# Kernel optimization log

Measured on AMD Instinct MI355X. Metric: run time of the kernel, lower is better.

Reference implementation:

```python
import jax, jax.numpy as jnp
import numpy as np

E, T, IN, OUT = 8, 16384, 1024, 1024  # n_groups, total_tokens, in_features, out_features


def setup_inputs() -> dict:
    key = jax.random.key(0)
    kx, kw, ks = jax.random.split(key, 3)
    x = jax.random.normal(kx, (T, IN), dtype=jnp.float32)
    # kaiming_uniform-ish scale for weight [E, OUT, IN]
    weight = jax.random.normal(kw, (E, OUT, IN), dtype=jnp.float32) * (1.0 / np.sqrt(IN))
    # ragged segment lengths that sum exactly to T (random cut points)
    cuts = jnp.sort(jax.random.randint(ks, (E - 1,), 0, T + 1)).astype(jnp.int32)
    seg_lens = jnp.diff(
        jnp.concatenate([jnp.zeros((1,), jnp.int32), cuts, jnp.full((1,), T, jnp.int32)])
    )
    return {"x": x, "weight": weight, "seg_lens": seg_lens}


def reference(x, weight, seg_lens):
    # Grouped GEMM: row t of x is multiplied by weight[g(t)].T where g(t) is the
    # segment (expert) that token t falls into per seg_lens. trans_b=True.
    n_groups = weight.shape[0]
    bounds = jnp.cumsum(seg_lens)                                  # [E]
    seg_id = jnp.searchsorted(bounds, jnp.arange(x.shape[0]), side="right")  # [T]
    y = jnp.zeros((x.shape[0], weight.shape[1]), dtype=x.dtype)
    for e in range(n_groups):  # small fixed loop over groups
        y = y + jnp.where((seg_id == e)[:, None], x @ weight[e].T, 0)
    return y
```

## Files before the change

### kernel.cpp

```cpp
#include <hip/hip_runtime.h>

#define T_TOK  16384
#define IN_F   1024
#define OUT_F  1024
#define NE     8

typedef __bf16 bf16;
typedef bf16  bf16x4 __attribute__((ext_vector_type(4)));
typedef bf16  bf16x8 __attribute__((ext_vector_type(8)));
typedef float f32x4  __attribute__((ext_vector_type(4)));

#define CVT_THREADS 256
#define NX_CHUNKS (T_TOK * IN_F / 4)
#define NW_CHUNKS (NE * OUT_F * IN_F / 4)
#define NTOT_CHUNKS (NX_CHUNKS + NW_CHUNKS)

__global__ __launch_bounds__(CVT_THREADS)
void cvt_f32_to_bf16(const float* __restrict__ x, const float* __restrict__ w,
                     bf16* __restrict__ xb, bf16* __restrict__ wb)
{
    for (int i = blockIdx.x * CVT_THREADS + threadIdx.x; i < NTOT_CHUNKS;
         i += gridDim.x * CVT_THREADS) {
        const bool isx = (i < NX_CHUNKS);
        const int  j   = isx ? i : i - NX_CHUNKS;
        f32x4 v = isx ? ((const f32x4*)x)[j] : ((const f32x4*)w)[j];
        bf16x4 h;
        #pragma unroll
        for (int k = 0; k < 4; ++k) h[k] = (bf16)v[k];
        if (isx) ((bf16x4*)xb)[j] = h;
        else     ((bf16x4*)wb)[j] = h;
    }
}

#define BM 256
#define BN 256
#define BK 64
#define GTHREADS 512
#define ROW_SLOTS 72

__device__ __forceinline__ void gld_lds16(const bf16* g, bf16* l) {
    __builtin_amdgcn_global_load_lds(
        (const __attribute__((address_space(1))) void*)g,
        (__attribute__((address_space(3))) void*)l,
        16, 0, 0);
}

__global__ __launch_bounds__(GTHREADS)
void grouped_gemm_bf16_256(const bf16* __restrict__ xb,
                           const bf16* __restrict__ wb,
                           const int*  __restrict__ seg_lens,
                           float* __restrict__ out)
{
    __shared__ __align__(16) bf16 As[2][BM * BK];
    __shared__ __align__(16) bf16 Bs[2][BN * BK];

    const int m    = blockIdx.y;
    const int col0 = blockIdx.x * BN;

    int e_sel = -1, row0 = 0, rows = 0;
    {
        int start = 0, acct = 0;
        #pragma unroll
        for (int e = 0; e < NE; ++e) {
            int len = seg_lens[e];
            int nt  = (len + BM - 1) >> 8;
            if (e_sel < 0 && m >= acct && m < acct + nt) {
                e_sel = e;
                row0  = start + (m - acct) * BM;
                int rem = start + len - row0;
                rows = rem < BM ? rem : BM;
            }
            acct  += nt;
            start += len;
        }
    }
    if (e_sel < 0) return;

    const int tid  = threadIdx.x;
    const int lane = tid & 63;
    const int wave = tid >> 6;
    const int wr   = wave >> 2;
    const int wc   = wave & 3;
    const int quad = lane >> 4;
    const int l16  = lane & 15;

    const bf16* wbase = wb + ((size_t)e_sel * OUT_F + (size_t)col0) * IN_F;

    const int rq = lane >> 3;
    const int ke = (lane & 7) * 8;
    const bf16* ga[4];
    const bf16* gb[4];
    #pragma unroll
    for (int i = 0; i < 4; ++i) {
        int q  = wave * 4 + i;
        int ra = row0 + q * 8 + rq;
        if (ra > T_TOK - 1) ra = T_TOK - 1;
        ga[i] = xb + (size_t)ra * IN_F + ke;
        gb[i] = wbase + (size_t)(q * 8 + rq) * IN_F + ke;
    }
    const int q0 = wave * 4;

    f32x4 acc[8][4] = {};

    #pragma unroll
    for (int i = 0; i < 4; ++i) {
        gld_lds16(ga[i], &As[0][(q0 + i) * 512]);
        gld_lds16(gb[i], &Bs[0][(q0 + i) * 512]);
    }
    __syncthreads();

    int cur = 0;
    for (int ks = 0; ks < IN_F / BK; ++ks) {
        const int kn = (ks + 1) * BK;
        if (kn < IN_F) {
            #pragma unroll
            for (int i = 0; i < 4; ++i) {
                gld_lds16(ga[i] + kn, &As[cur ^ 1][(q0 + i) * 512]);
                gld_lds16(gb[i] + kn, &Bs[cur ^ 1][(q0 + i) * 512]);
            }
        }

        #pragma unroll
        for (int kk = 0; kk < 2; ++kk) {
            bf16x8 af[8], bfr[4];
            #pragma unroll
            for (int t = 0; t < 8; ++t)
                af[t] = *(const bf16x8*)(
                    &As[cur][(wr * 128 + t * 16 + l16) * BK + kk * 32 + quad * 8]);
            #pragma unroll
            for (int u = 0; u < 4; ++u)
                bfr[u] = *(const bf16x8*)(
                    &Bs[cur][(wc * 64 + u * 16 + l16) * BK + kk * 32 + quad * 8]);
            #pragma unroll
            for (int t = 0; t < 8; ++t)
                #pragma unroll
                for (int u = 0; u < 4; ++u)
                    acc[t][u] = __builtin_amdgcn_mfma_f32_16x16x32_bf16(
                        af[t], bfr[u], acc[t][u], 0, 0, 0);
        }

        __syncthreads();
        cur ^= 1;
    }

    #pragma unroll
    for (int t = 0; t < 8; ++t) {
        #pragma unroll
        for (int r = 0; r < 4; ++r) {
            int row = wr * 128 + t * 16 + quad * 4 + r;
            if (row < rows) {
                size_t ob = (size_t)(row0 + row) * OUT_F + col0 + wc * 64;
                #pragma unroll
                for (int u = 0; u < 4; ++u)
                    out[ob + u * 16 + l16] = acc[t][u][r];
            }
        }
    }
}

#define FBM 128
#define FBK 32
#define FTHREADS 256
#define FROW_SLOTS 136

__global__ __launch_bounds__(FTHREADS)
void grouped_gemm_f32io_bf16(const float* __restrict__ x,
                             const float* __restrict__ wgt,
                             const int*  __restrict__ seg_lens,
                             float* __restrict__ out)
{
    __shared__ __align__(16) bf16 Asf[FBM * FBK];
    __shared__ __align__(16) bf16 Bsf[FBM * FBK];

    const int m    = blockIdx.y;
    const int col0 = blockIdx.x * FBM;

    int e_sel = -1, row0 = 0, rows = 0;
    {
        int start = 0, acct = 0;
        #pragma unroll
        for (int e = 0; e < NE; ++e) {
            int len = seg_lens[e];
            int nt  = (len + FBM - 1) >> 7;
            if (e_sel < 0 && m >= acct && m < acct + nt) {
                e_sel = e;
                row0  = start + (m - acct) * FBM;
                int rem = start + len - row0;
                rows = rem < FBM ? rem : FBM;
            }
            acct  += nt;
            start += len;
        }
    }
    if (e_sel < 0) return;

    const int tid  = threadIdx.x;
    const int lane = tid & 63;
    const int wave = tid >> 6;
    const int wm   = (wave >> 1) * 64;
    const int wn   = (wave & 1) * 64;
    const int quad = lane >> 4;
    const int l16  = lane & 15;

    const float* wbase = wgt + ((size_t)e_sel * OUT_F + (size_t)col0) * IN_F;

    f32x4 acc[4][4] = {};

    for (int k0 = 0; k0 < IN_F; k0 += FBK) {
        f32x4 a_st[4], b_st[4];
        #pragma unroll
        for (int t = 0; t < 4; ++t) {
            int c  = t * FTHREADS + tid;
            int rg = row0 + (c >> 3);
            if (rg > T_TOK - 1) rg = T_TOK - 1;
            a_st[t] = *(const f32x4*)(x + (size_t)rg * IN_F + k0 + (c & 7) * 4);
            b_st[t] = *(const f32x4*)(wbase + (size_t)(c >> 3) * IN_F + k0 + (c & 7) * 4);
        }

        __syncthreads();

        #pragma unroll
        for (int t = 0; t < 4; ++t) {
            int c = t * FTHREADS + tid;
            bf16x4 ha, hb;
            #pragma unroll
            for (int j = 0; j < 4; ++j) { ha[j] = (bf16)a_st[t][j]; hb[j] = (bf16)b_st[t][j]; }
            *(bf16x4*)(&Asf[(c >> 3) * FBK + (c & 7) * 4]) = ha;
            *(bf16x4*)(&Bsf[(c >> 3) * FBK + (c & 7) * 4]) = hb;
        }
        __syncthreads();

        bf16x8 af[4], bfr[4];
        #pragma unroll
        for (int t = 0; t < 4; ++t)
            af[t] = *(const bf16x8*)(&Asf[(wm + t * 16 + l16) * FBK + quad * 8]);
        #pragma unroll
        for (int u = 0; u < 4; ++u)
            bfr[u] = *(const bf16x8*)(&Bsf[(wn + u * 16 + l16) * FBK + quad * 8]);

        #pragma unroll
        for (int t = 0; t < 4; ++t)
            #pragma unroll
            for (int u = 0; u < 4; ++u)
                acc[t][u] = __builtin_amdgcn_mfma_f32_16x16x32_bf16(
                    af[t], bfr[u], acc[t][u], 0, 0, 0);
    }

    #pragma unroll
    for (int t = 0; t < 4; ++t) {
        #pragma unroll
        for (int r = 0; r < 4; ++r) {
            int row = wm + t * 16 + quad * 4 + r;
            if (row < rows) {
                size_t ob = (size_t)(row0 + row) * OUT_F + col0;
                #pragma unroll
                for (int u = 0; u < 4; ++u)
                    out[ob + wn + u * 16 + l16] = acc[t][u][r];
            }
        }
    }
}

extern "C" void kernel_launch(void* const* d_in, const int* in_sizes, int n_in,
                              void* d_out, int out_size, void* d_ws, size_t ws_size,
                              hipStream_t stream) {
    const float* x   = (const float*)d_in[0];
    const float* wgt = (const float*)d_in[1];
    const int*   seg = (const int*)d_in[2];
    float* out = (float*)d_out;

    const size_t xbytes = (size_t)T_TOK * IN_F * sizeof(bf16);
    const size_t wbytes = (size_t)NE * OUT_F * IN_F * sizeof(bf16);

    if (ws_size >= xbytes + wbytes) {
        bf16* xb = (bf16*)d_ws;
        bf16* wb = (bf16*)((char*)d_ws + xbytes);
        cvt_f32_to_bf16<<<dim3(2048, 1, 1), dim3(CVT_THREADS, 1, 1), 0, stream>>>(
            x, wgt, xb, wb);
        grouped_gemm_bf16_256<<<dim3(OUT_F / BN, ROW_SLOTS, 1),
                                dim3(GTHREADS, 1, 1), 0, stream>>>(xb, wb, seg, out);
    } else {
        grouped_gemm_f32io_bf16<<<dim3(OUT_F / FBM, FROW_SLOTS, 1),
                                  dim3(FTHREADS, 1, 1), 0, stream>>>(x, wgt, seg, out);
    }
}
```

Measured before the change: 232.1 us.

## Replace tiled grouped GEMM with stream-K scheduling over 256 persistent blocks

After: 235.4 us. No clear change (+1.4%).

```diff
diff --git a/kernel.cpp b/kernel.cpp
--- a/kernel.cpp
+++ b/kernel.cpp
@@ -13,22 +13,30 @@
 #define CVT_THREADS 256
 #define NX_CHUNKS (T_TOK * IN_F / 4)
 #define NW_CHUNKS (NE * OUT_F * IN_F / 4)
-#define NTOT_CHUNKS (NX_CHUNKS + NW_CHUNKS)
+#define NO_CHUNKS (T_TOK * OUT_F / 4)
+#define NCVT_CHUNKS (NX_CHUNKS + NW_CHUNKS)
+#define NALL_CHUNKS (NCVT_CHUNKS + NO_CHUNKS)
 
 __global__ __launch_bounds__(CVT_THREADS)
-void cvt_f32_to_bf16(const float* __restrict__ x, const float* __restrict__ w,
-                     bf16* __restrict__ xb, bf16* __restrict__ wb)
+void cvt_and_zero(const float* __restrict__ x, const float* __restrict__ w,
+                  bf16* __restrict__ xb, bf16* __restrict__ wb,
+                  float* __restrict__ out)
 {
-    for (int i = blockIdx.x * CVT_THREADS + threadIdx.x; i < NTOT_CHUNKS;
+    for (int i = blockIdx.x * CVT_THREADS + threadIdx.x; i < NALL_CHUNKS;
          i += gridDim.x * CVT_THREADS) {
-        const bool isx = (i < NX_CHUNKS);
-        const int  j   = isx ? i : i - NX_CHUNKS;
-        f32x4 v = isx ? ((const f32x4*)x)[j] : ((const f32x4*)w)[j];
-        bf16x4 h;
-        #pragma unroll
-        for (int k = 0; k < 4; ++k) h[k] = (bf16)v[k];
-        if (isx) ((bf16x4*)xb)[j] = h;
-        else     ((bf16x4*)wb)[j] = h;
+        if (i < NCVT_CHUNKS) {
+            const bool isx = (i < NX_CHUNKS);
+            const int  j   = isx ? i : i - NX_CHUNKS;
+            f32x4 v = isx ? ((const f32x4*)x)[j] : ((const f32x4*)w)[j];
+            bf16x4 h;
+            #pragma unroll
+            for (int k = 0; k < 4; ++k) h[k] = (bf16)v[k];
+            if (isx) ((bf16x4*)xb)[j] = h;
+            else     ((bf16x4*)wb)[j] = h;
+        } else {
+            f32x4 z = {0.f, 0.f, 0.f, 0.f};
+            ((f32x4*)out)[i - NCVT_CHUNKS] = z;
+        }
     }
 }
 
@@ -36,7 +44,8 @@
 #define BN 256
 #define BK 64
 #define GTHREADS 512
-#define ROW_SLOTS 72
+#define NBLOCKS 256
+#define KCH (IN_F / BK)
 
 __device__ __forceinline__ void gld_lds16(const bf16* g, bf16* l) {
     __builtin_amdgcn_global_load_lds(
@@ -46,35 +55,13 @@
 }
 
 __global__ __launch_bounds__(GTHREADS)
-void grouped_gemm_bf16_256(const bf16* __restrict__ xb,
-                           const bf16* __restrict__ wb,
-                           const int*  __restrict__ seg_lens,
-                           float* __restrict__ out)
+void grouped_gemm_streamk(const bf16* __restrict__ xb,
+                          const bf16* __restrict__ wb,
+                          const int*  __restrict__ seg_lens,
+                          float* __restrict__ out)
 {
     __shared__ __align__(16) bf16 As[2][BM * BK];
     __shared__ __align__(16) bf16 Bs[2][BN * BK];
-
-    const int m    = blockIdx.y;
-    const int col0 = blockIdx.x * BN;
-
-    int e_sel = -1, row0 = 0, rows = 0;
-    {
-        int start = 0, acct = 0;
-        #pragma unroll
-        for (int e = 0; e < NE; ++e) {
-            int len = seg_lens[e];
-            int nt  = (len + BM - 1) >> 8;
-            if (e_sel < 0 && m >= acct && m < acct + nt) {
-                e_sel = e;
-                row0  = start + (m - acct) * BM;
-                int rem = start + len - row0;
-                rows = rem < BM ? rem : BM;
-            }
-            acct  += nt;
-            start += len;
-        }
-    }
-    if (e_sel < 0) return;
 
     const int tid  = threadIdx.x;
     const int lane = tid & 63;
@@ -83,76 +70,140 @@
     const int wc   = wave & 3;
     const int quad = lane >> 4;
     const int l16  = lane & 15;
-
-    const bf16* wbase = wb + ((size_t)e_sel * OUT_F + (size_t)col0) * IN_F;
-
-    const int rq = lane >> 3;
-    const int ke = (lane & 7) * 8;
-    const bf16* ga[4];
-    const bf16* gb[4];
+    const int rq   = lane >> 3;
+    const int ke   = (lane & 7) * 8;
+    const int q0   = wave * 4;
+
+    int sl[NE];
     #pragma unroll
-    for (int i = 0; i < 4; ++i) {
-        int q  = wave * 4 + i;
-        int ra = row0 + q * 8 + rq;
-        if (ra > T_TOK - 1) ra = T_TOK - 1;
-        ga[i] = xb + (size_t)ra * IN_F + ke;
-        gb[i] = wbase + (size_t)(q * 8 + rq) * IN_F + ke;
-    }
-    const int q0 = wave * 4;
-
-    f32x4 acc[8][4] = {};
-
+    for (int e = 0; e < NE; ++e) sl[e] = seg_lens[e];
+
+    int n_slots = 0;
     #pragma unroll
-    for (int i = 0; i < 4; ++i) {
-        gld_lds16(ga[i], &As[0][(q0 + i) * 512]);
-        gld_lds16(gb[i], &Bs[0][(q0 + i) * 512]);
-    }
-    __syncthreads();
-
-    int cur = 0;
-    for (int ks = 0; ks < IN_F / BK; ++ks) {
-        const int kn = (ks + 1) * BK;
-        if (kn < IN_F) {
+    for (int e = 0; e < NE; ++e) n_slots += (sl[e] + BM - 1) >> 8;
+
+    const int L    = n_slots * (OUT_F / BN);
+    const int U    = L * KCH;
+    const int base = U >> 8;
+    const int rem  = U & 255;
+    const int b    = blockIdx.x;
+    int u          = b * base + (b < rem ? b : rem);
+    const int uend = u + base + (b < rem ? 1 : 0);
+
+    while (u < uend) {
+        const int tile = u >> 4;
+        const int kc0  = u & (KCH - 1);
+        int kc1 = kc0 + (uend - u);
+        if (kc1 > KCH) kc1 = KCH;
+        u += kc1 - kc0;
+
+        const int slot = tile >> 2;
+        const int col0 = (tile & 3) << 8;
+
+        int e_sel = -1, row0 = 0, rows = 0;
+        {
+            int start = 0, acct = 0;
+            #pragma unroll
+            for (int e = 0; e < NE; ++e) {
+                int len = sl[e];
+                int nt  = (len + BM - 1) >> 8;
+                if (e_sel < 0 && slot >= acct && slot < acct + nt) {
+                    e_sel = e;
+                    row0  = start + (slot - acct) * BM;
+                    int rm = start + len - row0;
+                    rows = rm < BM ? rm : BM;
+                }
+                acct  += nt;
+                start += len;
+            }
+        }
+
+        const bf16* wbase = wb + ((size_t)e_sel * OUT_F + (size_t)col0) * IN_F;
+
+        const bf16* ga[4];
+        const bf16* gb[4];
+        #pragma unroll
+        for (int i = 0; i < 4; ++i) {
+            int q  = wave * 4 + i;
+            int ra = row0 + q * 8 + rq;
+            if (ra > T_TOK - 1) ra = T_TOK - 1;
+            ga[i] = xb + (size_t)ra * IN_F + ke;
+            gb[i] = wbase + (size_t)(q * 8 + rq) * IN_F + ke;
+        }
+
+        f32x4 acc[8][4] = {};
+
+        {
+            const int kb = kc0 * BK;
             #pragma unroll
             for (int i = 0; i < 4; ++i) {
-                gld_lds16(ga[i] + kn, &As[cur ^ 1][(q0 + i) * 512]);
-                gld_lds16(gb[i] + kn, &Bs[cur ^ 1][(q0 + i) * 512]);
-            }
-        }
-
-        #pragma unroll
-        for (int kk = 0; kk < 2; ++kk) {
-            bf16x8 af[8], bfr[4];
-            #pragma unroll
-            for (int t = 0; t < 8; ++t)
-                af[t] = *(const bf16x8*)(
-                    &As[cur][(wr * 128 + t * 16 + l16) * BK + kk * 32 + quad * 8]);
-            #pragma unroll
-            for (int u = 0; u < 4; ++u)
-                bfr[u] = *(const bf16x8*)(
-                    &Bs[cur][(wc * 64 + u * 16 + l16) * BK + kk * 32 + quad * 8]);
-            #pragma unroll
-            for (int t = 0; t < 8; ++t)
-                #pragma unroll
-                for (int u = 0; u < 4; ++u)
-                    acc[t][u] = __builtin_amdgcn_mfma_f32_16x16x32_bf16(
-                        af[t], bfr[u], acc[t][u], 0, 0, 0);
-        }
-
+                gld_lds16(ga[i] + kb, &As[0][(q0 + i) * 512]);
+                gld_lds16(gb[i] + kb, &Bs[0][(q0 + i) * 512]);
+            }
+        }
         __syncthreads();
-        cur ^= 1;
-    }
-
-    #pragma unroll
-    for (int t = 0; t < 8; ++t) {
-        #pragma unroll
-        for (int r = 0; r < 4; ++r) {
-            int row = wr * 128 + t * 16 + quad * 4 + r;
-            if (row < rows) {
-                size_t ob = (size_t)(row0 + row) * OUT_F + col0 + wc * 64;
-                #pragma unroll
-                for (int u = 0; u < 4; ++u)
-                    out[ob + u * 16 + l16] = acc[t][u][r];
+
+        int cur = 0;
+        for (int ks = kc0; ks < kc1; ++ks) {
+            const int kn = (ks + 1) * BK;
+            if (ks + 1 < kc1) {
+                #pragma unroll
+                for (int i = 0; i < 4; ++i) {
+                    gld_lds16(ga[i] + kn, &As[cur ^ 1][(q0 + i) * 512]);
+                    gld_lds16(gb[i] + kn, &Bs[cur ^ 1][(q0 + i) * 512]);
+                }
+            }
+
+            #pragma unroll
+            for (int kk = 0; kk < 2; ++kk) {
+                bf16x8 af[8], bfr[4];
+                #pragma unroll
+                for (int t = 0; t < 8; ++t)
+                    af[t] = *(const bf16x8*)(
+                        &As[cur][(wr * 128 + t * 16 + l16) * BK + kk * 32 + quad * 8]);
+                #pragma unroll
+                for (int v = 0; v < 4; ++v)
+                    bfr[v] = *(const bf16x8*)(
+                        &Bs[cur][(wc * 64 + v * 16 + l16) * BK + kk * 32 + quad * 8]);
+                #pragma unroll
+                for (int t = 0; t < 8; ++t)
+                    #pragma unroll
+                    for (int v = 0; v < 4; ++v)
+                        acc[t][v] = __builtin_amdgcn_mfma_f32_16x16x32_bf16(
+                            af[t], bfr[v], acc[t][v], 0, 0, 0);
+            }
+
+            __syncthreads();
+            cur ^= 1;
+        }
+
+        if (kc0 == 0 && kc1 == KCH) {
+            #pragma unroll
+            for (int t = 0; t < 8; ++t) {
+                #pragma unroll
+                for (int r = 0; r < 4; ++r) {
+                    int row = wr * 128 + t * 16 + quad * 4 + r;
+                    if (row < rows) {
+                        size_t ob = (size_t)(row0 + row) * OUT_F + col0 + wc * 64;
+                        #pragma unroll
+                        for (int v = 0; v < 4; ++v)
+                            out[ob + v * 16 + l16] = acc[t][v][r];
+                    }
+                }
+            }
+        } else {
+            #pragma unroll
+            for (int t = 0; t < 8; ++t) {
+                #pragma unroll
+                for (int r = 0; r < 4; ++r) {
+                    int row = wr * 128 + t * 16 + quad * 4 + r;
+                    if (row < rows) {
+                        size_t ob = (size_t)(row0 + row) * OUT_F + col0 + wc * 64;
+                        #pragma unroll
+                        for (int v = 0; v < 4; ++v)
+                            unsafeAtomicAdd(&out[ob + v * 16 + l16], acc[t][v][r]);
+                    }
+                }
             }
         }
     }
@@ -235,15 +286,15 @@
         for (int t = 0; t < 4; ++t)
             af[t] = *(const bf16x8*)(&Asf[(wm + t * 16 + l16) * FBK + quad * 8]);
         #pragma unroll
-        for (int u = 0; u < 4; ++u)
-            bfr[u] = *(const bf16x8*)(&Bsf[(wn + u * 16 + l16) * FBK + quad * 8]);
+        for (int v = 0; v < 4; ++v)
+            bfr[v] = *(const bf16x8*)(&Bsf[(wn + v * 16 + l16) * FBK + quad * 8]);
 
         #pragma unroll
         for (int t = 0; t < 4; ++t)
             #pragma unroll
-            for (int u = 0; u < 4; ++u)
-                acc[t][u] = __builtin_amdgcn_mfma_f32_16x16x32_bf16(
-                    af[t], bfr[u], acc[t][u], 0, 0, 0);
+            for (int v = 0; v < 4; ++v)
+                acc[t][v] = __builtin_amdgcn_mfma_f32_16x16x32_bf16(
+                    af[t], bfr[v], acc[t][v], 0, 0, 0);
     }
 
     #pragma unroll
@@ -254,8 +305,8 @@
             if (row < rows) {
                 size_t ob = (size_t)(row0 + row) * OUT_F + col0;
                 #pragma unroll
-                for (int u = 0; u < 4; ++u)
-                    out[ob + wn + u * 16 + l16] = acc[t][u][r];
+                for (int v = 0; v < 4; ++v)
+                    out[ob + wn + v * 16 + l16] = acc[t][v][r];
             }
         }
     }
@@ -275,10 +326,10 @@
     if (ws_size >= xbytes + wbytes) {
         bf16* xb = (bf16*)d_ws;
         bf16* wb = (bf16*)((char*)d_ws + xbytes);
-        cvt_f32_to_bf16<<<dim3(2048, 1, 1), dim3(CVT_THREADS, 1, 1), 0, stream>>>(
-            x, wgt, xb, wb);
-        grouped_gemm_bf16_256<<<dim3(OUT_F / BN, ROW_SLOTS, 1),
-                                dim3(GTHREADS, 1, 1), 0, stream>>>(xb, wb, seg, out);
+        cvt_and_zero<<<dim3(2048, 1, 1), dim3(CVT_THREADS, 1, 1), 0, stream>>>(
+            x, wgt, xb, wb, out);
+        grouped_gemm_streamk<<<dim3(NBLOCKS, 1, 1), dim3(GTHREADS, 1, 1), 0, stream>>>(
+            xb, wb, seg, out);
     } else {
         grouped_gemm_f32io_bf16<<<dim3(OUT_F / FBM, FROW_SLOTS, 1),
                                   dim3(FTHREADS, 1, 1), 0, stream>>>(x, wgt, seg, out);
```
